# Kernel tuning notes

Hardware: AMD Instinct MI355X
Metric: run time of the kernel (lower is better)

Reference implementation:

```python
import jax, jax.numpy as jnp
import numpy as np

B, S, D_IN, D_MODEL, H = 4, 2048, 1024, 1024, 16
HD = D_MODEL // H  # head_dim = 64


def setup_inputs() -> dict:
    key = jax.random.key(0)
    ks = jax.random.split(key, 9)
    scale = 1.0 / np.sqrt(D_IN)
    return {
        "Q": jax.random.normal(ks[0], (B, S, D_IN), jnp.float32),
        "V": jax.random.normal(ks[1], (B, S, D_IN), jnp.float32),
        "K": jax.random.normal(ks[2], (B, S, D_IN), jnp.float32),
        "wq": jax.random.uniform(ks[3], (D_IN, D_MODEL), jnp.float32, -scale, scale),
        "bq": jax.random.uniform(ks[4], (D_MODEL,), jnp.float32, -scale, scale),
        "wk": jax.random.uniform(ks[5], (D_IN, D_MODEL), jnp.float32, -scale, scale),
        "bk": jax.random.uniform(ks[6], (D_MODEL,), jnp.float32, -scale, scale),
        "wv": jax.random.uniform(ks[7], (D_IN, D_MODEL), jnp.float32, -scale, scale),
        "bv": jax.random.uniform(ks[8], (D_MODEL,), jnp.float32, -scale, scale),
    }


def _split_heads(x):
    # [B,S,D] -> [B,H,S,HD]
    return x.reshape(B, S, H, HD).transpose(0, 2, 1, 3)


def reference(Q, V, K, wq, bq, wk, bk, wv, bv):
    q = _split_heads(Q @ wq + bq)
    k = _split_heads(K @ wk + bk)
    v = _split_heads(V @ wv + bv)
    scores = jnp.einsum("bhqd,bhkd->bhqk", q, k) / jnp.sqrt(jnp.float32(HD))
    weights = jax.nn.softmax(scores, axis=-1)
    out = jnp.einsum("bhqk,bhkd->bhqd", weights, v)
    return out.transpose(0, 2, 1, 3).reshape(B, S, D_MODEL)
```

## Files before the change

### kernel.cpp

```cpp
#include <hip/hip_runtime.h>
#include <hip/hip_bf16.h>

typedef unsigned short u16;
typedef __attribute__((ext_vector_type(8))) short bf16x8;
typedef __attribute__((ext_vector_type(4))) float f32x4;
typedef __attribute__((ext_vector_type(16))) float f32x16;
typedef __attribute__((ext_vector_type(4))) unsigned short u16x4;
typedef __attribute__((ext_vector_type(2))) unsigned u32x2;

#define NB 4
#define NS 2048
#define DIN 1024
#define DM 1024
#define NH 16
#define HD 64
#define LOG2E 1.44269504f

__device__ __forceinline__ u16 f2bf(float f) {
  union { float f; unsigned u; } x; x.f = f;
  unsigned r = x.u + 0x7fffu + ((x.u >> 16) & 1u);
  return (u16)(r >> 16);
}

__device__ __forceinline__ unsigned pk_bf16(float a, float b) {
  union { __hip_bfloat162 h; unsigned u; } cv;
  cv.h = __float22bfloat162_rn(make_float2(a, b));
  return cv.u;
}

__device__ __forceinline__ void gl_lds16(const u16* g, u16* l) {
  __builtin_amdgcn_global_load_lds((const __attribute__((address_space(1))) void*)g,
                                   (__attribute__((address_space(3))) void*)l, 16, 0, 0);
}

__global__ void prep_kernel(const float* __restrict__ Qp, const float* __restrict__ Kp,
                            const float* __restrict__ Vp, u16* __restrict__ oq,
                            u16* __restrict__ ok, u16* __restrict__ ov,
                            const float* __restrict__ wqp, const float* __restrict__ wkp,
                            const float* __restrict__ wvp, u16* __restrict__ owq,
                            u16* __restrict__ owk, u16* __restrict__ owv, int n4) {
  __shared__ float tile[64][65];
  const int b = blockIdx.x, t = threadIdx.x;
  if (b < 3072) {
    const int ten = b >> 10, bx = b & 1023;
    const float* s = ten == 0 ? Qp : ten == 1 ? Kp : Vp;
    u16* d = ten == 0 ? oq : ten == 1 ? ok : ov;
    int stride = 1024 * 256;
    for (int i = bx * 256 + t; i < n4; i += stride) {
      f32x4 v = ((const f32x4*)s)[i];
      u32x2 o;
      o.x = pk_bf16(v.x, v.y);
      o.y = pk_bf16(v.z, v.w);
      ((u32x2*)d)[i] = o;
    }
  } else {
    const int wt = b - 3072;
    const int z = wt >> 8, rem = wt & 255;
    const float* W = z == 0 ? wqp : z == 1 ? wkp : wvp;
    u16* Wt = z == 0 ? owq : z == 1 ? owk : owv;
    int n0 = (rem & 15) * 64, k0 = (rem >> 4) * 64;
#pragma unroll
    for (int i = 0; i < 16; i++) {
      int idx = t + i * 256;
      int r = idx >> 6, c = idx & 63;
      tile[r][c] = W[(size_t)(k0 + r) * DM + n0 + c];
    }
    __syncthreads();
#pragma unroll
    for (int i = 0; i < 16; i++) {
      int idx = t + i * 256;
      int r = idx >> 6, c = idx & 63;
      Wt[(size_t)(n0 + r) * DIN + k0 + c] = f2bf(tile[c][r]);
    }
  }
}

__global__ __launch_bounds__(256) void proj_kernel(
    const u16* __restrict__ Xq, const u16* __restrict__ Xk, const u16* __restrict__ Xv,
    const u16* __restrict__ Wtq, const u16* __restrict__ Wtk, const u16* __restrict__ Wtv,
    const float* __restrict__ bq, const float* __restrict__ bk, const float* __restrict__ bv,
    u16* __restrict__ oq, u16* __restrict__ ok, u16* __restrict__ ov) {
  __shared__ __align__(16) u16 Abuf[128 * 64];
  __shared__ __align__(16) u16 Bbuf[128 * 64];
  const int bid = blockIdx.x;
  const int xr = bid & 7;
  const int nt = (bid >> 3) & 7;
  const int mt = (bid >> 6) & 7;
  const int z  = bid >> 9;
  const int m0 = (mt * 8 + xr) * 128, n0 = nt * 128;
  const u16* X  = z == 0 ? Xq : z == 1 ? Xk : Xv;
  const u16* Wt = z == 0 ? Wtq : z == 1 ? Wtk : Wtv;
  const float* bias = z == 0 ? bq : z == 1 ? bk : bv;
  u16* out = z == 0 ? oq : z == 1 ? ok : ov;
  const int t = threadIdx.x, lane = t & 63, w = t >> 6;
  const int c = lane & 15, g = lane >> 4;
  const int wm = (w >> 1) * 64, wn = (w & 1) * 64;
  f32x4 acc[4][4] = {};
  for (int k0 = 0; k0 < DIN; k0 += 64) {
#pragma unroll
    for (int i = 0; i < 4; i++) {
      int idx = (w * 4 + i) * 64 + lane;
      int row = idx >> 3;
      int srck = (idx & 7) ^ (row & 7);
      gl_lds16(&X [(size_t)(m0 + row) * DIN + k0 + srck * 8], &Abuf[(w * 4 + i) * 512]);
      gl_lds16(&Wt[(size_t)(n0 + row) * DIN + k0 + srck * 8], &Bbuf[(w * 4 + i) * 512]);
    }
    __syncthreads();
#pragma unroll
    for (int ks = 0; ks < 2; ks++) {
      bf16x8 xf[4], wf[4];
      int chn = ((ks * 4 + g) ^ (c & 7)) * 8;
#pragma unroll
      for (int a = 0; a < 4; a++) {
        xf[a] = *(const bf16x8*)&Abuf[(wm + a * 16 + c) * 64 + chn];
        wf[a] = *(const bf16x8*)&Bbuf[(wn + a * 16 + c) * 64 + chn];
      }
      if (z < 2) {
#pragma unroll
        for (int i = 0; i < 4; i++)
#pragma unroll
          for (int j = 0; j < 4; j++)
            acc[i][j] = __builtin_amdgcn_mfma_f32_16x16x32_bf16(wf[i], xf[j], acc[i][j], 0, 0, 0);
      } else {
#pragma unroll
        for (int i = 0; i < 4; i++)
#pragma unroll
          for (int j = 0; j < 4; j++)
            acc[i][j] = __builtin_amdgcn_mfma_f32_16x16x32_bf16(xf[i], wf[j], acc[i][j], 0, 0, 0);
      }
    }
    __syncthreads();
  }
  if (z < 2) {
    const float sc = (z == 0) ? 0.125f * LOG2E : 1.0f;
#pragma unroll
    for (int i = 0; i < 4; i++) {
      int nb = n0 + wn + i * 16 + g * 4;
      int h = nb >> 6, d0 = nb & 63;
      f32x4 bv4 = *(const f32x4*)&bias[nb];
#pragma unroll
      for (int j = 0; j < 4; j++) {
        int mm = m0 + wm + j * 16 + c;
        int b = mm >> 11, s = mm & 2047;
        u16x4 pk;
#pragma unroll
        for (int r = 0; r < 4; r++) pk[r] = f2bf((acc[i][j][r] + bv4[r]) * sc);
        *(u16x4*)&out[((size_t)(b * NH + h) * NS + s) * HD + d0] = pk;
      }
    }
  } else {
#pragma unroll
    for (int j = 0; j < 4; j++) {
      int n = n0 + wn + j * 16 + c;
      int h = n >> 6, d = n & 63;
      float bvs = bias[n];
#pragma unroll
      for (int i = 0; i < 4; i++) {
        int mb = m0 + wm + i * 16 + g * 4;
        int b = mb >> 11, s0 = mb & 2047;
        u16x4 pk;
#pragma unroll
        for (int r = 0; r < 4; r++) pk[r] = f2bf(acc[i][j][r] + bvs);
        *(u16x4*)&out[((size_t)(b * NH + h) * HD + d) * NS + s0] = pk;
      }
    }
  }
}

__global__ __launch_bounds__(256, 2) void attn_kernel(
    const u16* __restrict__ q, const u16* __restrict__ k, const u16* __restrict__ vT,
    float* __restrict__ out) {
  __shared__ __align__(16) u16 kt[64 * 64];
  __shared__ __align__(16) u16 vt[64 * 64];
  const int bid = blockIdx.x;
  const int xr = bid & 7;
  const int qc = (bid >> 3) & 15;
  const int h8 = bid >> 7;
  const int bh = xr + 8 * h8;
  const int t = threadIdx.x, lane = t & 63, w = t >> 6;
  const int h = lane >> 5, ql = lane & 31, c7 = lane & 7;
  const int q0 = qc * 128 + w * 32;
  const u16* qsrc = q + ((size_t)bh * NS + q0) * HD;
  const u16* ksrc = k + (size_t)bh * NS * HD;
  const u16* vsrc = vT + (size_t)bh * HD * NS;
  const int srow = lane >> 3;
  const int skc = (lane & 7) ^ srow;
  bf16x8 qf[4];
#pragma unroll
  for (int ks = 0; ks < 4; ks++)
    qf[ks] = *(const bf16x8*)&qsrc[ql * HD + ks * 16 + h * 8];
  f32x16 o32[2] = {};
  float lacc = 0.f;
  for (int kt0 = 0; kt0 < NS; kt0 += 64) {
#pragma unroll
    for (int j = 0; j < 2; j++) {
      int row = w * 16 + j * 8 + srow;
      gl_lds16(&ksrc[(size_t)(kt0 + row) * HD + skc * 8], &kt[(w * 16 + j * 8) * 64]);
      gl_lds16(&vsrc[(size_t)row * NS + kt0 + skc * 8], &vt[(w * 16 + j * 8) * 64]);
    }
    __syncthreads();
#pragma unroll
    for (int kb = 0; kb < 2; kb++) {
      f32x16 s32 = {};
      __builtin_amdgcn_s_setprio(1);
#pragma unroll
      for (int ks = 0; ks < 4; ks++) {
        bf16x8 ka = *(const bf16x8*)&kt[(kb * 32 + ql) * 64 + (((ks * 2 + h) ^ c7) * 8)];
        s32 = __builtin_amdgcn_mfma_f32_32x32x16_bf16(ka, qf[ks], s32, 0, 0, 0);
      }
      __builtin_amdgcn_s_setprio(0);
      float e[16];
#pragma unroll
      for (int r = 0; r < 16; r++) e[r] = __builtin_amdgcn_exp2f(s32[r]);
      {
        float t0 = (e[0] + e[1]) + (e[2] + e[3]);
        float t1 = (e[4] + e[5]) + (e[6] + e[7]);
        float t2 = (e[8] + e[9]) + (e[10] + e[11]);
        float t3 = (e[12] + e[13]) + (e[14] + e[15]);
        lacc += (t0 + t1) + (t2 + t3);
      }
#pragma unroll
      for (int s = 0; s < 2; s++) {
        unsigned A  = pk_bf16(e[8 * s + 0], e[8 * s + 1]);
        unsigned Bp = pk_bf16(e[8 * s + 2], e[8 * s + 3]);
        unsigned C  = pk_bf16(e[8 * s + 4], e[8 * s + 5]);
        unsigned D  = pk_bf16(e[8 * s + 6], e[8 * s + 7]);
        u32x2 r02 = __builtin_amdgcn_permlane32_swap(A, C, false, false);
        u32x2 r13 = __builtin_amdgcn_permlane32_swap(Bp, D, false, false);
        union { unsigned u[4]; bf16x8 v; } pf;
        pf.u[0] = r02.x; pf.u[1] = r13.x; pf.u[2] = r02.y; pf.u[3] = r13.y;
        const int ksl = kb * 2 + s;
        __builtin_amdgcn_s_setprio(1);
#pragma unroll
        for (int db = 0; db < 2; db++) {
          bf16x8 va = *(const bf16x8*)&vt[(db * 32 + ql) * 64 + (((ksl * 2 + h) ^ c7) * 8)];
          o32[db] = __builtin_amdgcn_mfma_f32_32x32x16_bf16(va, pf.v, o32[db], 0, 0, 0);
        }
        __builtin_amdgcn_s_setprio(0);
      }
    }
    __syncthreads();
  }
  const float lq = lacc + __shfl_xor(lacc, 32);
  const float inv = 1.f / lq;
  const int b = bh >> 4, hh = bh & 15;
  const int s_idx = q0 + ql;
  float* obase = &out[((size_t)b * NS + s_idx) * DM + hh * HD];
#pragma unroll
  for (int db = 0; db < 2; db++)
#pragma unroll
    for (int i = 0; i < 4; i++) {
      f32x4 ov = { o32[db][4 * i + 0] * inv, o32[db][4 * i + 1] * inv,
                   o32[db][4 * i + 2] * inv, o32[db][4 * i + 3] * inv };
      *(f32x4*)&obase[db * 32 + 8 * i + 4 * h] = ov;
    }
}

extern "C" void kernel_launch(void* const* d_in, const int* in_sizes, int n_in,
                              void* d_out, int out_size, void* d_ws, size_t ws_size,
                              hipStream_t stream) {
  const float* Q  = (const float*)d_in[0];
  const float* V  = (const float*)d_in[1];
  const float* K  = (const float*)d_in[2];
  const float* wq = (const float*)d_in[3];
  const float* bq = (const float*)d_in[4];
  const float* wk = (const float*)d_in[5];
  const float* bk = (const float*)d_in[6];
  const float* wv = (const float*)d_in[7];
  const float* bv = (const float*)d_in[8];
  float* out = (float*)d_out;
  char* ws = (char*)d_ws;
  const size_t NX = (size_t)NB * NS * DIN;
  const size_t XB = NX * 2;
  const size_t WB = (size_t)DIN * DM * 2;
  u16* Xq   = (u16*)(ws);
  u16* Xk   = (u16*)(ws + XB);
  u16* Xv   = (u16*)(ws + 2 * XB);
  u16* Wtq  = (u16*)(ws + 3 * XB);
  u16* Wtk  = (u16*)(ws + 3 * XB + WB);
  u16* Wtv  = (u16*)(ws + 3 * XB + 2 * WB);
  u16* qws  = (u16*)(ws + 3 * XB + 3 * WB);
  u16* kws  = (u16*)(ws + 4 * XB + 3 * WB);
  u16* vTws = (u16*)(ws + 5 * XB + 3 * WB);
  const int n4 = (int)(NX / 4);
  prep_kernel<<<3840, 256, 0, stream>>>(Q, K, V, Xq, Xk, Xv,
                                        wq, wk, wv, Wtq, Wtk, Wtv, n4);
  proj_kernel<<<1536, 256, 0, stream>>>(Xq, Xk, Xv, Wtq, Wtk, Wtv,
                                        bq, bk, bv, qws, kws, vTws);
  attn_kernel<<<1024, 256, 0, stream>>>(qws, kws, vTws, out);
}
```

Measured before the change: 304.4 us.

## Split attention key range across two blocks and combine partial results

The attention grid is doubled so each block handles half of the key sequence. Each block writes unnormalized partial outputs and row sums to separate buffers. A new combine kernel then adds the two partials and normalizes them. The aim is more parallelism and better CU fill, paid for with an extra kernel launch and roughly 100 MB of extra fp32 global traffic.

Result: slower. 319.7 us (+5.0%).

```diff
diff --git a/kernel.cpp b/kernel.cpp
--- a/kernel.cpp
+++ b/kernel.cpp
@@ -169,13 +169,15 @@
 
 __global__ __launch_bounds__(256, 2) void attn_kernel(
     const u16* __restrict__ q, const u16* __restrict__ k, const u16* __restrict__ vT,
-    float* __restrict__ out) {
+    float* __restrict__ out, float* __restrict__ O1,
+    float* __restrict__ l0p, float* __restrict__ l1p) {
   __shared__ __align__(16) u16 kt[64 * 64];
   __shared__ __align__(16) u16 vt[64 * 64];
   const int bid = blockIdx.x;
   const int xr = bid & 7;
   const int qc = (bid >> 3) & 15;
-  const int h8 = bid >> 7;
+  const int h8 = (bid >> 7) & 7;
+  const int hv = bid >> 10;
   const int bh = xr + 8 * h8;
   const int t = threadIdx.x, lane = t & 63, w = t >> 6;
   const int h = lane >> 5, ql = lane & 31, c7 = lane & 7;
@@ -191,7 +193,8 @@
     qf[ks] = *(const bf16x8*)&qsrc[ql * HD + ks * 16 + h * 8];
   f32x16 o32[2] = {};
   float lacc = 0.f;
-  for (int kt0 = 0; kt0 < NS; kt0 += 64) {
+  const int kbeg = hv * 1024;
+  for (int kt0 = kbeg; kt0 < kbeg + 1024; kt0 += 64) {
 #pragma unroll
     for (int j = 0; j < 2; j++) {
       int row = w * 16 + j * 8 + srow;
@@ -242,18 +245,34 @@
     __syncthreads();
   }
   const float lq = lacc + __shfl_xor(lacc, 32);
-  const float inv = 1.f / lq;
   const int b = bh >> 4, hh = bh & 15;
   const int s_idx = q0 + ql;
-  float* obase = &out[((size_t)b * NS + s_idx) * DM + hh * HD];
+  float* obase = (hv ? O1 : out) + ((size_t)b * NS + s_idx) * DM + hh * HD;
 #pragma unroll
   for (int db = 0; db < 2; db++)
 #pragma unroll
     for (int i = 0; i < 4; i++) {
-      f32x4 ov = { o32[db][4 * i + 0] * inv, o32[db][4 * i + 1] * inv,
-                   o32[db][4 * i + 2] * inv, o32[db][4 * i + 3] * inv };
+      f32x4 ov = { o32[db][4 * i + 0], o32[db][4 * i + 1],
+                   o32[db][4 * i + 2], o32[db][4 * i + 3] };
       *(f32x4*)&obase[db * 32 + 8 * i + 4 * h] = ov;
     }
+  if (h == 0) (hv ? l1p : l0p)[(size_t)bh * NS + s_idx] = lq;
+}
+
+__global__ __launch_bounds__(256) void combine_kernel(
+    float* __restrict__ out, const float* __restrict__ O1,
+    const float* __restrict__ l0, const float* __restrict__ l1) {
+  const int i = blockIdx.x * 256 + threadIdx.x;
+  const int head = (i >> 4) & 15;
+  const int s = (i >> 8) & 2047;
+  const int b = i >> 19;
+  const size_t li = (size_t)(b * NH + head) * NS + s;
+  const float inv = 1.f / (l0[li] + l1[li]);
+  f32x4 a = ((const f32x4*)out)[i];
+  f32x4 c = ((const f32x4*)O1)[i];
+  f32x4 r = { (a.x + c.x) * inv, (a.y + c.y) * inv,
+              (a.z + c.z) * inv, (a.w + c.w) * inv };
+  ((f32x4*)out)[i] = r;
 }
 
 extern "C" void kernel_launch(void* const* d_in, const int* in_sizes, int n_in,
@@ -282,10 +301,14 @@
   u16* qws  = (u16*)(ws + 3 * XB + 3 * WB);
   u16* kws  = (u16*)(ws + 4 * XB + 3 * WB);
   u16* vTws = (u16*)(ws + 5 * XB + 3 * WB);
+  float* O1p = (float*)(ws);
+  float* l0p = (float*)(ws + 32 * 1024 * 1024);
+  float* l1p = (float*)(ws + 32 * 1024 * 1024 + 512 * 1024);
   const int n4 = (int)(NX / 4);
   prep_kernel<<<3840, 256, 0, stream>>>(Q, K, V, Xq, Xk, Xv,
                                         wq, wk, wv, Wtq, Wtk, Wtv, n4);
   proj_kernel<<<1536, 256, 0, stream>>>(Xq, Xk, Xv, Wtq, Wtk, Wtv,
                                         bq, bk, bv, qws, kws, vTws);
-  attn_kernel<<<1024, 256, 0, stream>>>(qws, kws, vTws, out);
-}
+  attn_kernel<<<2048, 256, 0, stream>>>(qws, kws, vTws, out, O1p, l0p, l1p);
+  combine_kernel<<<8192, 256, 0, stream>>>(out, O1p, l0p, l1p);
+}
```

## Double-buffer K/V tiles in attention kernel with prefetch of next tile

Applied to the files above, without the earlier changes.

The attention kernel gets two LDS buffers each for K and V. The next 64-key tile is prefetched with direct global-to-LDS loads while the current tile is computed, using partial vmcnt waits and raw barriers instead of __syncthreads. This aims to hide global load latency behind the MFMA and softmax work. It doubles LDS use per block to 32KB, which could limit occupancy at 2 blocks per CU, and it relies on hand-placed waitcnt for correctness.

Measured after the change: 311.4 us. +2.3%, slower.

```diff
diff --git a/kernel.cpp b/kernel.cpp
--- a/kernel.cpp
+++ b/kernel.cpp
@@ -170,8 +170,8 @@
 __global__ __launch_bounds__(256, 2) void attn_kernel(
     const u16* __restrict__ q, const u16* __restrict__ k, const u16* __restrict__ vT,
     float* __restrict__ out) {
-  __shared__ __align__(16) u16 kt[64 * 64];
-  __shared__ __align__(16) u16 vt[64 * 64];
+  __shared__ __align__(16) u16 kt[2][64 * 64];
+  __shared__ __align__(16) u16 vt[2][64 * 64];
   const int bid = blockIdx.x;
   const int xr = bid & 7;
   const int qc = (bid >> 3) & 15;
@@ -191,21 +191,38 @@
     qf[ks] = *(const bf16x8*)&qsrc[ql * HD + ks * 16 + h * 8];
   f32x16 o32[2] = {};
   float lacc = 0.f;
+
+#define STAGE(buf, kk0)                                                            \
+  {                                                                                \
+    _Pragma("unroll") for (int j = 0; j < 2; j++) {                                \
+      int row = w * 16 + j * 8 + srow;                                             \
+      gl_lds16(&ksrc[(size_t)((kk0) + row) * HD + skc * 8],                        \
+               &kt[buf][(w * 16 + j * 8) * 64]);                                   \
+      gl_lds16(&vsrc[(size_t)row * NS + (kk0) + skc * 8],                          \
+               &vt[buf][(w * 16 + j * 8) * 64]);                                   \
+    }                                                                              \
+  }
+
+  STAGE(0, 0);
+  int cur = 0;
   for (int kt0 = 0; kt0 < NS; kt0 += 64) {
-#pragma unroll
-    for (int j = 0; j < 2; j++) {
-      int row = w * 16 + j * 8 + srow;
-      gl_lds16(&ksrc[(size_t)(kt0 + row) * HD + skc * 8], &kt[(w * 16 + j * 8) * 64]);
-      gl_lds16(&vsrc[(size_t)row * NS + kt0 + skc * 8], &vt[(w * 16 + j * 8) * 64]);
-    }
-    __syncthreads();
+    if (kt0 + 64 < NS) {
+      STAGE(cur ^ 1, kt0 + 64);
+      asm volatile("s_waitcnt vmcnt(4)" ::: "memory");
+    } else {
+      asm volatile("s_waitcnt vmcnt(0)" ::: "memory");
+    }
+    __builtin_amdgcn_s_barrier();
+    __builtin_amdgcn_sched_barrier(0);
+    const u16* ktc = kt[cur];
+    const u16* vtc = vt[cur];
 #pragma unroll
     for (int kb = 0; kb < 2; kb++) {
       f32x16 s32 = {};
       __builtin_amdgcn_s_setprio(1);
 #pragma unroll
       for (int ks = 0; ks < 4; ks++) {
-        bf16x8 ka = *(const bf16x8*)&kt[(kb * 32 + ql) * 64 + (((ks * 2 + h) ^ c7) * 8)];
+        bf16x8 ka = *(const bf16x8*)&ktc[(kb * 32 + ql) * 64 + (((ks * 2 + h) ^ c7) * 8)];
         s32 = __builtin_amdgcn_mfma_f32_32x32x16_bf16(ka, qf[ks], s32, 0, 0, 0);
       }
       __builtin_amdgcn_s_setprio(0);
@@ -233,14 +250,18 @@
         __builtin_amdgcn_s_setprio(1);
 #pragma unroll
         for (int db = 0; db < 2; db++) {
-          bf16x8 va = *(const bf16x8*)&vt[(db * 32 + ql) * 64 + (((ksl * 2 + h) ^ c7) * 8)];
+          bf16x8 va = *(const bf16x8*)&vtc[(db * 32 + ql) * 64 + (((ksl * 2 + h) ^ c7) * 8)];
           o32[db] = __builtin_amdgcn_mfma_f32_32x32x16_bf16(va, pf.v, o32[db], 0, 0, 0);
         }
         __builtin_amdgcn_s_setprio(0);
       }
     }
-    __syncthreads();
-  }
+    asm volatile("s_waitcnt lgkmcnt(0)" ::: "memory");
+    __builtin_amdgcn_s_barrier();
+    __builtin_amdgcn_sched_barrier(0);
+    cur ^= 1;
+  }
+#undef STAGE
   const float lq = lacc + __shfl_xor(lacc, 32);
   const float inv = 1.f / lq;
   const int b = bh >> 4, hh = bh & 15;
```
